# Performance work log

Measured on AMD Instinct MI355X. Metric: run time of the kernel, lower is better.

## Reference

```python
import jax, jax.numpy as jnp
import numpy as np


def setup_inputs() -> dict:
    key = jax.random.key(0)
    ks = jax.random.split(key, 6)
    B, S, D, E = 4, 2048, 1024, 8
    H = 4 * D
    return {
        "x": jax.random.normal(ks[0], (B, S, D), dtype=jnp.float32),
        "logits": jax.random.normal(ks[1], (B, S, E), dtype=jnp.float32),
        "noise": jax.random.normal(ks[2], (B, S, E), dtype=jnp.float32),
        "W1": jax.random.normal(ks[3], (E, D, H), dtype=jnp.float32) * (1.0 / np.sqrt(D)),
        "b1": jnp.zeros((E, H), dtype=jnp.float32),
        "W2": jax.random.normal(ks[4], (E, H, D), dtype=jnp.float32) * (1.0 / np.sqrt(H)),
        "b2": jnp.zeros((E, D), dtype=jnp.float32),
        "top_k": 2,
    }


def reference(x, logits, noise, W1, b1, W2, b2, top_k):
    # NoisyTopkRouter_Cluster: noise scaled by softplus(logits), then sparse top-k softmax
    B, S, D = x.shape
    E = logits.shape[-1]
    noisy = logits + noise * jax.nn.softplus(logits)           # [B,S,E]
    _, topi = jax.lax.top_k(noisy, top_k)                      # [B,S,K]
    in_topk = jax.nn.one_hot(topi, E, dtype=jnp.bool_).any(-2)  # [B,S,E]
    sparse = jnp.where(in_topk, noisy, -jnp.inf)
    gates = jax.nn.softmax(sparse, axis=-1)                    # [B,S,E]; zero off top-k

    # SparseMoE combine: sum_e gate[:, e] * Expert_e(x). Gate is exactly 0 for
    # unselected experts, so dense-masked compute matches the gather/scatter loop.
    xf = x.reshape(-1, D)                                      # [T,D]
    gf = gates.reshape(-1, E).T                                # [E,T]

    def body(acc, params):
        w1, bb1, w2, bb2, g = params                           # g: [T]
        h = jax.nn.relu(xf @ w1 + bb1)                         # [T,4D]
        acc = acc + (h @ w2 + bb2) * g[:, None]
        return acc, None

    acc, _ = jax.lax.scan(body, jnp.zeros_like(xf), (W1, b1, W2, b2, gf))
    return acc.reshape(B, S, D)
```

## Files before the change

kernel.cpp:

```cpp
#include <hip/hip_runtime.h>
#include <cstdint>
#include <cstddef>

#define T_TOK 8192
#define E_NUM 8
#define D_DIM 1024
#define H_DIM 4096
#define MAXTILES 72
#define TILE 256
#define BK 32
#define STAGES 3

typedef __attribute__((ext_vector_type(8))) short short8;
typedef __attribute__((ext_vector_type(4))) float f32x4;
typedef __attribute__((ext_vector_type(8))) unsigned short ushort8v;
typedef __attribute__((ext_vector_type(4))) unsigned short ushort4v;

__device__ __forceinline__ unsigned short f2b(float f) {
  unsigned int u = __float_as_uint(f);
  u += 0x7fffu + ((u >> 16) & 1u);
  return (unsigned short)(u >> 16);
}

__device__ __forceinline__ void async16(const void* g, void* l) {
  __builtin_amdgcn_global_load_lds((const __attribute__((address_space(1))) void*)g,
                                   (__attribute__((address_space(3))) void*)l, 16, 0, 0);
}

__global__ void router_kernel(const float* __restrict__ logits, const float* __restrict__ noise,
                              int* __restrict__ counts, int* __restrict__ ti, float* __restrict__ tg) {
  int tk = blockIdx.x * blockDim.x + threadIdx.x;
  if (tk >= T_TOK) return;
  float nz[E_NUM];
#pragma unroll
  for (int e = 0; e < E_NUM; ++e) {
    float l = logits[tk * E_NUM + e];
    float sp = fmaxf(l, 0.f) + log1pf(expf(-fabsf(l)));
    nz[e] = l + noise[tk * E_NUM + e] * sp;
  }
  int i1 = 0; float v1 = nz[0];
#pragma unroll
  for (int e = 1; e < E_NUM; ++e) if (nz[e] > v1) { v1 = nz[e]; i1 = e; }
  int i2 = -1; float v2 = -3.0e38f;
#pragma unroll
  for (int e = 0; e < E_NUM; ++e) if (e != i1 && nz[e] > v2) { v2 = nz[e]; i2 = e; }
  float ex = expf(v2 - v1);
  float g1 = 1.f / (1.f + ex);
  float g2 = ex / (1.f + ex);
  int s1 = atomicAdd(&counts[i1], 1);
  int s2 = atomicAdd(&counts[i2], 1);
  ti[tk*4+0] = i1; ti[tk*4+1] = s1; ti[tk*4+2] = i2; ti[tk*4+3] = s2;
  tg[tk*2+0] = g1; tg[tk*2+1] = g2;
}

__global__ void setup_kernel(const int* __restrict__ counts, int* __restrict__ offs,
                             int* __restrict__ tab) {
  int o = 0;
  for (int e = 0; e < E_NUM; ++e) { offs[e] = o; o += counts[e]; }
  offs[E_NUM] = o;
  int mt = 0;
  for (int e = 0; e < E_NUM; ++e)
    for (int m0 = 0; m0 < counts[e]; m0 += TILE) { tab[mt*2] = e; tab[mt*2+1] = m0; ++mt; }
  for (; mt < MAXTILES; ++mt) { tab[mt*2] = -1; tab[mt*2+1] = 0; }
}

__global__ void gather_kernel(const float* __restrict__ x, const int* __restrict__ ti,
                              const float* __restrict__ tg, const int* __restrict__ offs,
                              unsigned short* __restrict__ xg, int* __restrict__ stok,
                              float* __restrict__ sg) {
  const int tk = blockIdx.x, t = threadIdx.x;
  const int i1 = ti[tk*4+0], s1 = ti[tk*4+1], i2 = ti[tk*4+2], s2 = ti[tk*4+3];
  const int r1 = offs[i1] + s1, r2 = offs[i2] + s2;
  if (t == 0) {
    stok[r1] = tk; sg[r1] = tg[tk*2+0];
    stok[r2] = tk; sg[r2] = tg[tk*2+1];
  }
  const float4 v = *(const float4*)(x + (size_t)tk * D_DIM + t * 4);
  ushort4v bb; bb.x = f2b(v.x); bb.y = f2b(v.y); bb.z = f2b(v.z); bb.w = f2b(v.w);
  *(ushort4v*)(xg + (size_t)r1 * D_DIM + t * 4) = bb;
  *(ushort4v*)(xg + (size_t)r2 * D_DIM + t * 4) = bb;
}

__global__ void transpose_kernel(const float* __restrict__ W, unsigned short* __restrict__ Wt,
                                 int K, int N) {
  const int e = blockIdx.z;
  const float* We = W + (size_t)e * K * N;
  unsigned short* Wte = Wt + (size_t)e * K * N;
  __shared__ __align__(16) unsigned short tb[64 * 72];
  const int n0 = blockIdx.x * 64, k0 = blockIdx.y * 64;
  const int t = threadIdx.x;
  const int kr = t >> 4;
  const int c4 = (t & 15) * 4;
#pragma unroll
  for (int rr = 0; rr < 4; ++rr) {
    int k = kr + rr * 16;
    const float4 v = *(const float4*)(We + (size_t)(k0 + k) * N + n0 + c4);
    tb[(c4+0)*72 + k] = f2b(v.x);
    tb[(c4+1)*72 + k] = f2b(v.y);
    tb[(c4+2)*72 + k] = f2b(v.z);
    tb[(c4+3)*72 + k] = f2b(v.w);
  }
  __syncthreads();
  const int n = t >> 2, kq = (t & 3) * 16;
  ushort8v a = *(const ushort8v*)&tb[n*72 + kq];
  ushort8v b = *(const ushort8v*)&tb[n*72 + kq + 8];
  *(ushort8v*)(Wte + (size_t)(n0+n)*K + k0 + kq) = a;
  *(ushort8v*)(Wte + (size_t)(n0+n)*K + k0 + kq + 8) = b;
}

template<int EPI, int NX, int KSPLIT>
__global__ __launch_bounds__(512, 2)
void gemm_bt(const unsigned short* __restrict__ A, const unsigned short* __restrict__ Bt,
             const int K, const int N,
             const int* __restrict__ counts, const int* __restrict__ offs,
             const int* __restrict__ tab,
             const float* __restrict__ bias,
             unsigned short* __restrict__ Hout,
             float* __restrict__ Out,
             const int* __restrict__ slot_tok, const float* __restrict__ slot_gate) {
  constexpr int GRID = NX * MAXTILES * KSPLIT;
  constexpr int Q = GRID / 8;
  const int bid = blockIdx.x;
  const int lin = (bid & 7) * Q + (bid >> 3);
  const int mt  = lin % MAXTILES;
  const int u   = lin / MAXTILES;
  const int kb  = u % KSPLIT;
  const int xi  = u / KSPLIT;

  const int e = tab[mt*2];
  if (e < 0) return;
  const int m0  = tab[mt*2+1];
  const int cnt = counts[e];
  const int seg = offs[e];
  const int n0  = xi * TILE;
  const int KC  = K / KSPLIT;
  const int ks  = kb * KC;
  const int kend = ks + KC;

  __shared__ __align__(16) short smem[STAGES * 2 * TILE * BK];
  __shared__ int   s_tok[TILE];
  __shared__ float s_g[TILE];

  const int t = threadIdx.x;
  const int lane = t & 63;
  const int wv = t >> 6;
  const int wm = wv >> 2, wn = wv & 3;
  const int fr = lane & 15, fq = lane >> 4;

  if (EPI == 1 && t < TILE) {
    int rl = m0 + t;
    if (rl < cnt) { s_tok[t] = slot_tok[seg + rl]; s_g[t] = slot_gate[seg + rl]; }
    else          { s_tok[t] = 0;                  s_g[t] = 0.f; }
  }
  __syncthreads();

  const unsigned short* Ae = A + (size_t)seg * K;
  const unsigned short* Be = Bt + (size_t)e * N * K + (size_t)n0 * K;

  const int rt = t >> 2;
  const int kc = (((t & 3) - (t >> 3)) & 3) * 8;
  int ar0 = m0 + rt;         ar0 = ar0 < cnt ? ar0 : cnt - 1;
  int ar1 = m0 + 128 + rt;   ar1 = ar1 < cnt ? ar1 : cnt - 1;
  const unsigned short* rA0 = Ae + (size_t)ar0 * K + kc;
  const unsigned short* rA1 = Ae + (size_t)ar1 * K + kc;
  const unsigned short* rB0 = Be + (size_t)rt * K + kc;
  const unsigned short* rB1 = Be + (size_t)(128 + rt) * K + kc;
  const int ldsW = wv * 1024;

  auto issue = [&](int ksh, int soff) {
    char* pA = (char*)smem + soff + ldsW;
    char* pB = (char*)smem + soff + 16384 + ldsW;
    async16(rA0 + ksh, pA);
    async16(rA1 + ksh, pA + 8192);
    async16(rB0 + ksh, pB);
    async16(rB1 + ksh, pB + 8192);
  };

  f32x4 acc[8][4];
#pragma unroll
  for (int i = 0; i < 8; ++i)
#pragma unroll
    for (int j = 0; j < 4; ++j) acc[i][j] = (f32x4){0.f, 0.f, 0.f, 0.f};

  issue(ks + 0 * BK, 0 * 32768);
  issue(ks + 1 * BK, 1 * 32768);
  issue(ks + 2 * BK, 2 * 32768);

  const int csw = ((fq + (fr >> 1)) & 3) * 8;

  int soff = 0;
  for (int k0 = ks; k0 < kend; k0 += BK) {
    asm volatile("s_waitcnt vmcnt(8)" ::: "memory");
    asm volatile("s_barrier" ::: "memory");

    const short* As = (const short*)((const char*)smem + soff);
    const short* Bs = (const short*)((const char*)smem + soff + 16384);
    short8 bfv[4];
#pragma unroll
    for (int j = 0; j < 4; ++j)
      bfv[j] = *(const short8*)&Bs[(wn*64 + j*16 + fr)*BK + csw];
#pragma unroll
    for (int i = 0; i < 8; ++i) {
      short8 af = *(const short8*)&As[(wm*128 + i*16 + fr)*BK + csw];
#pragma unroll
      for (int j = 0; j < 4; ++j)
        acc[i][j] = __builtin_amdgcn_mfma_f32_16x16x32_bf16(af, bfv[j], acc[i][j], 0, 0, 0);
    }

    asm volatile("s_barrier" ::: "memory");

    int kpre = k0 + STAGES * BK;
    if (kpre > kend - BK) kpre = kend - BK;
    issue(kpre, soff);
    soff += 32768; if (soff == STAGES * 32768) soff = 0;
  }

  if (EPI == 0) {
    const float* be = bias + (size_t)e * N;
#pragma unroll
    for (int j = 0; j < 4; ++j) {
      int col = n0 + wn*64 + j*16 + fr;
      float bv = be[col];
#pragma unroll
      for (int i = 0; i < 8; ++i) {
        int tl0 = wm*128 + i*16 + fq*4;
#pragma unroll
        for (int r = 0; r < 4; ++r) {
          int tlr = tl0 + r;
          if (m0 + tlr < cnt) {
            float v = acc[i][j][r] + bv;
            v = v > 0.f ? v : 0.f;
            Hout[(size_t)(seg + m0 + tlr) * N + col] = f2b(v);
          }
        }
      }
    }
  } else {
    const float* be = bias + (size_t)e * N;
#pragma unroll
    for (int j = 0; j < 4; ++j) {
      int col = n0 + wn*64 + j*16 + fr;
      float bv = (kb == 0) ? be[col] : 0.f;
#pragma unroll
      for (int i = 0; i < 8; ++i) {
        int tl0 = wm*128 + i*16 + fq*4;
#pragma unroll
        for (int r = 0; r < 4; ++r) {
          int tlr = tl0 + r;
          if (m0 + tlr < cnt) {
            float v = (acc[i][j][r] + bv) * s_g[tlr];
            unsafeAtomicAdd(Out + (size_t)s_tok[tlr] * N + col, v);
          }
        }
      }
    }
  }
}

extern "C" void kernel_launch(void* const* d_in, const int* in_sizes, int n_in,
                              void* d_out, int out_size, void* d_ws, size_t ws_size,
                              hipStream_t stream) {
  const float* x      = (const float*)d_in[0];
  const float* logits = (const float*)d_in[1];
  const float* noise  = (const float*)d_in[2];
  const float* W1     = (const float*)d_in[3];
  const float* b1     = (const float*)d_in[4];
  const float* W2     = (const float*)d_in[5];
  const float* b2     = (const float*)d_in[6];
  float* out = (float*)d_out;

  char* ws = (char*)d_ws;
  size_t off = 0;
  auto alloc = [&](size_t b) { size_t o = off; off = (off + b + 255) & ~(size_t)255; return o; };
  size_t o_counts = alloc(E_NUM * 4);
  size_t o_offs   = alloc((E_NUM + 1) * 4);
  size_t o_tab    = alloc((size_t)MAXTILES * 2 * 4);
  size_t o_ti     = alloc((size_t)T_TOK * 4 * 4);
  size_t o_tg     = alloc((size_t)T_TOK * 2 * 4);
  size_t o_stok   = alloc((size_t)2 * T_TOK * 4);
  size_t o_sg     = alloc((size_t)2 * T_TOK * 4);
  size_t o_xg     = alloc((size_t)2 * T_TOK * D_DIM * 2);
  size_t o_w1t    = alloc((size_t)E_NUM * D_DIM * H_DIM * 2);
  size_t o_w2t    = alloc((size_t)E_NUM * D_DIM * H_DIM * 2);
  size_t o_h      = alloc((size_t)2 * T_TOK * H_DIM * 2);
  if (off > ws_size) return;

  int*            counts = (int*)(ws + o_counts);
  int*            offsp  = (int*)(ws + o_offs);
  int*            tab    = (int*)(ws + o_tab);
  int*            ti     = (int*)(ws + o_ti);
  float*          tg     = (float*)(ws + o_tg);
  int*            stok   = (int*)(ws + o_stok);
  float*          sg     = (float*)(ws + o_sg);
  unsigned short* xg     = (unsigned short*)(ws + o_xg);
  unsigned short* w1t    = (unsigned short*)(ws + o_w1t);
  unsigned short* w2t    = (unsigned short*)(ws + o_w2t);
  unsigned short* h      = (unsigned short*)(ws + o_h);

  hipMemsetAsync(out, 0, (size_t)out_size * sizeof(float), stream);
  hipMemsetAsync(counts, 0, E_NUM * sizeof(int), stream);

  router_kernel<<<T_TOK / 256, 256, 0, stream>>>(logits, noise, counts, ti, tg);
  setup_kernel<<<1, 1, 0, stream>>>(counts, offsp, tab);
  gather_kernel<<<T_TOK, 256, 0, stream>>>(x, ti, tg, offsp, xg, stok, sg);

  transpose_kernel<<<dim3(H_DIM/64, D_DIM/64, E_NUM), 256, 0, stream>>>(W1, w1t, D_DIM, H_DIM);
  transpose_kernel<<<dim3(D_DIM/64, H_DIM/64, E_NUM), 256, 0, stream>>>(W2, w2t, H_DIM, D_DIM);

  gemm_bt<0, H_DIM/TILE, 1><<<dim3((H_DIM/TILE) * MAXTILES * 1), 512, 0, stream>>>(
      xg, w1t, D_DIM, H_DIM, counts, offsp, tab, b1, h, nullptr, nullptr, nullptr);
  gemm_bt<1, D_DIM/TILE, 4><<<dim3((D_DIM/TILE) * MAXTILES * 4), 512, 0, stream>>>(
      h, w2t, H_DIM, D_DIM, counts, offsp, tab, b2, nullptr, out, stok, sg);
}
```

Measured before the change: 1.085 ms.

## Rework grouped GEMM main loop into 8-phase ping-pong schedule with BK=64

```diff
diff --git a/kernel.cpp b/kernel.cpp
--- a/kernel.cpp
+++ b/kernel.cpp
@@ -8,8 +8,6 @@
 #define H_DIM 4096
 #define MAXTILES 72
 #define TILE 256
-#define BK 32
-#define STAGES 3
 
 typedef __attribute__((ext_vector_type(8))) short short8;
 typedef __attribute__((ext_vector_type(4))) float f32x4;
@@ -110,14 +108,14 @@
 
 template<int EPI, int NX, int KSPLIT>
 __global__ __launch_bounds__(512, 2)
-void gemm_bt(const unsigned short* __restrict__ A, const unsigned short* __restrict__ Bt,
-             const int K, const int N,
-             const int* __restrict__ counts, const int* __restrict__ offs,
-             const int* __restrict__ tab,
-             const float* __restrict__ bias,
-             unsigned short* __restrict__ Hout,
-             float* __restrict__ Out,
-             const int* __restrict__ slot_tok, const float* __restrict__ slot_gate) {
+void gemm8p(const unsigned short* __restrict__ A, const unsigned short* __restrict__ Bt,
+            const int K, const int N,
+            const int* __restrict__ counts, const int* __restrict__ offs,
+            const int* __restrict__ tab,
+            const float* __restrict__ bias,
+            unsigned short* __restrict__ Hout,
+            float* __restrict__ Out,
+            const int* __restrict__ slot_tok, const float* __restrict__ slot_gate) {
   constexpr int GRID = NX * MAXTILES * KSPLIT;
   constexpr int Q = GRID / 8;
   const int bid = blockIdx.x;
@@ -134,10 +132,10 @@
   const int seg = offs[e];
   const int n0  = xi * TILE;
   const int KC  = K / KSPLIT;
+  const int NT  = KC / 64;
   const int ks  = kb * KC;
-  const int kend = ks + KC;
-
-  __shared__ __align__(16) short smem[STAGES * 2 * TILE * BK];
+
+  __shared__ __align__(16) short smem[2 * 32768];
   __shared__ int   s_tok[TILE];
   __shared__ float s_g[TILE];
 
@@ -157,24 +155,42 @@
   const unsigned short* Ae = A + (size_t)seg * K;
   const unsigned short* Be = Bt + (size_t)e * N * K + (size_t)n0 * K;
 
-  const int rt = t >> 2;
-  const int kc = (((t & 3) - (t >> 3)) & 3) * 8;
-  int ar0 = m0 + rt;         ar0 = ar0 < cnt ? ar0 : cnt - 1;
-  int ar1 = m0 + 128 + rt;   ar1 = ar1 < cnt ? ar1 : cnt - 1;
-  const unsigned short* rA0 = Ae + (size_t)ar0 * K + kc;
-  const unsigned short* rA1 = Ae + (size_t)ar1 * K + kc;
-  const unsigned short* rB0 = Be + (size_t)rt * K + kc;
-  const unsigned short* rB1 = Be + (size_t)(128 + rt) * K + kc;
-  const int ldsW = wv * 1024;
-
-  auto issue = [&](int ksh, int soff) {
-    char* pA = (char*)smem + soff + ldsW;
-    char* pB = (char*)smem + soff + 16384 + ldsW;
-    async16(rA0 + ksh, pA);
-    async16(rA1 + ksh, pA + 8192);
-    async16(rB0 + ksh, pB);
-    async16(rB1 + ksh, pB + 8192);
+  const int rl   = wv * 8 + (lane >> 3);
+  const int swSt = ((lane & 7) ^ (lane >> 3)) * 8;
+  int am0 = m0 + rl;        am0 = am0 < cnt ? am0 : cnt - 1;
+  int am1 = m0 + rl + 64;   am1 = am1 < cnt ? am1 : cnt - 1;
+  int am2 = m0 + rl + 128;  am2 = am2 < cnt ? am2 : cnt - 1;
+  int am3 = m0 + rl + 192;  am3 = am3 < cnt ? am3 : cnt - 1;
+  const unsigned short* pa0 = Ae + (size_t)am0 * K + swSt;
+  const unsigned short* pa1 = Ae + (size_t)am1 * K + swSt;
+  const unsigned short* pa2 = Ae + (size_t)am2 * K + swSt;
+  const unsigned short* pa3 = Ae + (size_t)am3 * K + swSt;
+  const unsigned short* pb0 = Be + (size_t)(rl)       * K + swSt;
+  const unsigned short* pb1 = Be + (size_t)(rl + 64)  * K + swSt;
+  const unsigned short* pb2 = Be + (size_t)(rl + 128) * K + swSt;
+  const unsigned short* pb3 = Be + (size_t)(rl + 192) * K + swSt;
+  const int wvOff = wv * 1024;
+
+  auto issueA0 = [&](int par, int ko) {
+    char* d = (char*)smem + par * 65536 + wvOff;
+    async16(pa0 + ko, d); async16(pa1 + ko, d + 8192);
   };
+  auto issueA1 = [&](int par, int ko) {
+    char* d = (char*)smem + par * 65536 + 16384 + wvOff;
+    async16(pa2 + ko, d); async16(pa3 + ko, d + 8192);
+  };
+  auto issueB0 = [&](int par, int ko) {
+    char* d = (char*)smem + par * 65536 + 32768 + wvOff;
+    async16(pb0 + ko, d); async16(pb1 + ko, d + 8192);
+  };
+  auto issueB1 = [&](int par, int ko) {
+    char* d = (char*)smem + par * 65536 + 49152 + wvOff;
+    async16(pb2 + ko, d); async16(pb3 + ko, d + 8192);
+  };
+
+  const int sw0 = ((0 * 4 + fq) ^ (fr & 7)) * 8;
+  const int sw1 = ((1 * 4 + fq) ^ (fr & 7)) * 8;
+  const int bl  = (wn & 1) * 64;
 
   f32x4 acc[8][4];
 #pragma unroll
@@ -182,37 +198,99 @@
 #pragma unroll
     for (int j = 0; j < 4; ++j) acc[i][j] = (f32x4){0.f, 0.f, 0.f, 0.f};
 
-  issue(ks + 0 * BK, 0 * 32768);
-  issue(ks + 1 * BK, 1 * 32768);
-  issue(ks + 2 * BK, 2 * 32768);
-
-  const int csw = ((fq + (fr >> 1)) & 3) * 8;
-
-  int soff = 0;
-  for (int k0 = ks; k0 < kend; k0 += BK) {
-    asm volatile("s_waitcnt vmcnt(8)" ::: "memory");
-    asm volatile("s_barrier" ::: "memory");
-
-    const short* As = (const short*)((const char*)smem + soff);
-    const short* Bs = (const short*)((const char*)smem + soff + 16384);
-    short8 bfv[4];
-#pragma unroll
-    for (int j = 0; j < 4; ++j)
-      bfv[j] = *(const short8*)&Bs[(wn*64 + j*16 + fr)*BK + csw];
-#pragma unroll
-    for (int i = 0; i < 8; ++i) {
-      short8 af = *(const short8*)&As[(wm*128 + i*16 + fr)*BK + csw];
-#pragma unroll
-      for (int j = 0; j < 4; ++j)
-        acc[i][j] = __builtin_amdgcn_mfma_f32_16x16x32_bf16(af, bfv[j], acc[i][j], 0, 0, 0);
-    }
-
-    asm volatile("s_barrier" ::: "memory");
-
-    int kpre = k0 + STAGES * BK;
-    if (kpre > kend - BK) kpre = kend - BK;
-    issue(kpre, soff);
-    soff += 32768; if (soff == STAGES * 32768) soff = 0;
+  issueB0(0, ks); issueB1(0, ks);
+  issueA0(0, ks); issueA1(0, ks);
+  issueB0(1, ks + 64); issueB1(1, ks + 64);
+  asm volatile("s_waitcnt vmcnt(4)" ::: "memory");
+  asm volatile("s_barrier" ::: "memory");
+
+  short8 aLo[4][2], aHi[4][2], b01[2][2], b23[2][2];
+
+  for (int kt = 0; kt < NT; ++kt) {
+    const short* bR = smem + (kt & 1) * 32768;
+    const short* Aw = bR + wm * 8192;
+    const short* Bw = bR + 16384 + (wn >> 1) * 8192;
+    const int parA = (kt + 1) & 1, parB = kt & 1;
+    int tA = kt + 1; if (tA > NT - 1) tA = NT - 1;
+    int tB = kt + 2; if (tB > NT - 1) tB = NT - 1;
+    const int kA = ks + tA * 64, kB = ks + tB * 64;
+
+#pragma unroll
+    for (int i = 0; i < 4; ++i) {
+      int ro = (i * 16 + fr) * 64;
+      aLo[i][0] = *(const short8*)&Aw[ro + sw0];
+      aLo[i][1] = *(const short8*)&Aw[ro + sw1];
+    }
+#pragma unroll
+    for (int j = 0; j < 2; ++j) {
+      int ro = (bl + j * 16 + fr) * 64;
+      b01[j][0] = *(const short8*)&Bw[ro + sw0];
+      b01[j][1] = *(const short8*)&Bw[ro + sw1];
+    }
+    issueA0(parA, kA);
+    asm volatile("s_barrier" ::: "memory");
+    __builtin_amdgcn_s_setprio(1);
+#pragma unroll
+    for (int i = 0; i < 4; ++i)
+#pragma unroll
+      for (int j = 0; j < 2; ++j) {
+        acc[i][j] = __builtin_amdgcn_mfma_f32_16x16x32_bf16(aLo[i][0], b01[j][0], acc[i][j], 0, 0, 0);
+        acc[i][j] = __builtin_amdgcn_mfma_f32_16x16x32_bf16(aLo[i][1], b01[j][1], acc[i][j], 0, 0, 0);
+      }
+    __builtin_amdgcn_s_setprio(0);
+    asm volatile("s_barrier" ::: "memory");
+
+#pragma unroll
+    for (int j = 0; j < 2; ++j) {
+      int ro = (bl + 32 + j * 16 + fr) * 64;
+      b23[j][0] = *(const short8*)&Bw[ro + sw0];
+      b23[j][1] = *(const short8*)&Bw[ro + sw1];
+    }
+    issueA1(parA, kA);
+    asm volatile("s_barrier" ::: "memory");
+    __builtin_amdgcn_s_setprio(1);
+#pragma unroll
+    for (int i = 0; i < 4; ++i)
+#pragma unroll
+      for (int j = 0; j < 2; ++j) {
+        acc[i][j+2] = __builtin_amdgcn_mfma_f32_16x16x32_bf16(aLo[i][0], b23[j][0], acc[i][j+2], 0, 0, 0);
+        acc[i][j+2] = __builtin_amdgcn_mfma_f32_16x16x32_bf16(aLo[i][1], b23[j][1], acc[i][j+2], 0, 0, 0);
+      }
+    __builtin_amdgcn_s_setprio(0);
+    asm volatile("s_barrier" ::: "memory");
+
+#pragma unroll
+    for (int i = 0; i < 4; ++i) {
+      int ro = ((i + 4) * 16 + fr) * 64;
+      aHi[i][0] = *(const short8*)&Aw[ro + sw0];
+      aHi[i][1] = *(const short8*)&Aw[ro + sw1];
+    }
+    issueB0(parB, kB);
+    asm volatile("s_barrier" ::: "memory");
+    __builtin_amdgcn_s_setprio(1);
+#pragma unroll
+    for (int i = 0; i < 4; ++i)
+#pragma unroll
+      for (int j = 0; j < 2; ++j) {
+        acc[i+4][j+2] = __builtin_amdgcn_mfma_f32_16x16x32_bf16(aHi[i][0], b23[j][0], acc[i+4][j+2], 0, 0, 0);
+        acc[i+4][j+2] = __builtin_amdgcn_mfma_f32_16x16x32_bf16(aHi[i][1], b23[j][1], acc[i+4][j+2], 0, 0, 0);
+      }
+    __builtin_amdgcn_s_setprio(0);
+    asm volatile("s_barrier" ::: "memory");
+
+    issueB1(parB, kB);
+    asm volatile("s_barrier" ::: "memory");
+    __builtin_amdgcn_s_setprio(1);
+#pragma unroll
+    for (int i = 0; i < 4; ++i)
+#pragma unroll
+      for (int j = 0; j < 2; ++j) {
+        acc[i+4][j] = __builtin_amdgcn_mfma_f32_16x16x32_bf16(aHi[i][0], b01[j][0], acc[i+4][j], 0, 0, 0);
+        acc[i+4][j] = __builtin_amdgcn_mfma_f32_16x16x32_bf16(aHi[i][1], b01[j][1], acc[i+4][j], 0, 0, 0);
+      }
+    __builtin_amdgcn_s_setprio(0);
+    asm volatile("s_waitcnt vmcnt(4)" ::: "memory");
+    asm volatile("s_barrier" ::: "memory");
   }
 
   if (EPI == 0) {
@@ -307,8 +385,8 @@
   transpose_kernel<<<dim3(H_DIM/64, D_DIM/64, E_NUM), 256, 0, stream>>>(W1, w1t, D_DIM, H_DIM);
   transpose_kernel<<<dim3(D_DIM/64, H_DIM/64, E_NUM), 256, 0, stream>>>(W2, w2t, H_DIM, D_DIM);
 
-  gemm_bt<0, H_DIM/TILE, 1><<<dim3((H_DIM/TILE) * MAXTILES * 1), 512, 0, stream>>>(
+  gemm8p<0, H_DIM/TILE, 1><<<dim3((H_DIM/TILE) * MAXTILES * 1), 512, 0, stream>>>(
       xg, w1t, D_DIM, H_DIM, counts, offsp, tab, b1, h, nullptr, nullptr, nullptr);
-  gemm_bt<1, D_DIM/TILE, 4><<<dim3((D_DIM/TILE) * MAXTILES * 4), 512, 0, stream>>>(
+  gemm8p<1, D_DIM/TILE, 2><<<dim3((D_DIM/TILE) * MAXTILES * 2), 512, 0, stream>>>(
       h, w2t, H_DIM, D_DIM, counts, offsp, tab, b2, nullptr, out, stok, sg);
 }
```

Result: faster. 972.6 us (-10.4%).
